# Performance work log

Hardware: AMD Instinct MI355X
Metric: run time of the kernel (lower is better)

Reference implementation:

```python
import jax, jax.numpy as jnp
import numpy as np

S = 4  # spixel_downsize


def _shift2d(x, oy, ox):
    # out[..., y, x] = x[..., y - oy, x - ox] if in-bounds else 0 (zero pad)
    pad = [(0, 0)] * (x.ndim - 2) + [(S, S), (S, S)]
    xp = jnp.pad(x, pad)
    h, w = x.shape[-2], x.shape[-1]
    return xp[..., S - oy:S - oy + h, S - ox:S - ox + w]


def _valid_mask(h, w, oy, ox):
    ys = jnp.arange(h)
    xs = jnp.arange(w)
    my = (ys - oy >= 0) & (ys - oy < h)
    mx = (xs - ox >= 0) & (xs - ox < w)
    return my[:, None] & mx[None, :]


def _conv3d(x, w, stride, pad):
    return jax.lax.conv_general_dilated(
        x, w, window_strides=stride, padding=[(p, p) for p in pad],
        dimension_numbers=('NCDHW', 'OIDHW', 'NCDHW'))


def _basic(x, w, stride, pad):
    # BasicConv: Conv3d(bias=False) + BN(identity at init) + ReLU
    return jax.nn.relu(_conv3d(x, w, stride, pad))


def setup_inputs() -> dict:
    key = jax.random.key(0)
    ks = jax.random.split(key, 8)
    cv = jax.random.normal(ks[0], (1, 8, 24, 128, 256), jnp.float32)
    sp = jax.random.uniform(ks[1], (1, 9, 128, 256), jnp.float32)
    xy = jax.random.normal(ks[2], (1, 2, 128, 256), jnp.float32)
    w_stem = jax.random.normal(ks[3], (16, 72, 1, 1, 1), jnp.float32) * 0.05
    w1a = jax.random.normal(ks[4], (32, 16, 3, 2, 2), jnp.float32) * 0.05
    w1b = jax.random.normal(ks[5], (32, 32, 3, 1, 1), jnp.float32) * 0.05
    w2a = jax.random.normal(ks[6], (64, 32, 3, 2, 2), jnp.float32) * 0.05
    w2b = jax.random.normal(ks[7], (64, 64, 3, 1, 1), jnp.float32) * 0.05
    return dict(cv=cv, sp=sp, xy=xy, w_stem=w_stem, w1a=w1a, w1b=w1b, w2a=w2a, w2b=w2b)


def reference(cv, sp, xy, w_stem, w1a, w1b, w2a, w2b):
    b, c, d, h, w = cv.shape
    feats, probs = [], []
    uv0 = jnp.zeros((b, 2, h, w), cv.dtype)
    # 9 shifted neighbors; neighbor k shifts by (S*((k//3)-1), S*((k%3)-1)).
    # All uv writes in the original target slot 0 and sequentially overwrite;
    for k in range(9):
        oy = S * ((k // 3) - 1)
        ox = S * ((k % 3) - 1)
        p = _shift2d(sp[:, k], oy, ox)                      # (b,h,w), zeros outside
        probs.append(p)
        feats.append(_shift2d(cv, oy, ox) * p[:, None, None])  # (b,c,d,h,w)
        u = _shift2d(xy, oy, ox) * p[:, None]               # (b,2,h,w)
        mask = _valid_mask(h, w, oy, ox)[None, None]
        uv0 = jnp.where(mask, u, uv0)
    # (b, c, 9, d, h, w) -> (b, 9c, d, h, w), matching torch reshape order
    feat = jnp.stack(feats, axis=2).reshape(b, c * 9, d, h, w)
    prob_sum = jnp.sum(jnp.stack(probs, axis=1), axis=1, keepdims=True)  # (b,1,h,w)
    tot = prob_sum.reshape(b, 1, h // S, S, w // S, S).mean((3, 5))      # avg_pool2d
    tot_up = jnp.repeat(jnp.repeat(tot, S, axis=2), S, axis=3)           # nearest upsample
    feat = feat / tot_up[:, :, None]                                     # (b,9c,d,h,w)
    feat = _basic(feat, w_stem, (1, 1, 1), (0, 0, 0))
    f1 = _basic(feat, w1a, (2, 2, 2), (1, 0, 0))
    f1 = _basic(f1, w1b, (1, 1, 1), (1, 0, 0))
    f2 = _basic(f1, w2a, (2, 2, 2), (1, 0, 0))
    f2 = _basic(f2, w2b, (1, 1, 1), (1, 0, 0))
    # uv.sum(2) == uv0 since only neighbor-slot 0 is written
    uv = uv0.reshape(b, 2, h // S, S, w // S, S).mean((3, 5)) / tot      # (b,2,h/S,w/S)
    return f1, f2, uv.reshape(b, 2, -1)
```

## Files before the change

### kernel.cpp

```cpp
#include <hip/hip_runtime.h>

#define HH 128
#define WW 256
#define HW (HH * WW)

#define OFF_TOT   0
#define OFF_WT    2048
#define WT_STEM   0
#define WT_1A     1152
#define WT_1B     7296
#define WT_2A     10368
#define WT_2B     34944
#define OFF_STEM  49280
#define OFF_F1A   12632192
#define OFF_F1N   15777920
#define OFF_F2A   49280

__global__ __launch_bounds__(256) void k_pre(
    const float* __restrict__ sp, const float* __restrict__ xy,
    const float* __restrict__ wstem, const float* __restrict__ w1a,
    const float* __restrict__ w1b, const float* __restrict__ w2a,
    const float* __restrict__ w2b,
    float* __restrict__ tot, float* __restrict__ uv_out, float* __restrict__ wt)
{
  int gid = blockIdx.x * 256 + threadIdx.x;
  if (gid < 1152) { int o = gid & 15, r = gid >> 4; int ci = r / 9, k = r - ci * 9;
    wt[WT_STEM + gid] = wstem[o * 72 + ci * 9 + k]; }
  if (gid < 6144) { int o = gid & 31, ci = (gid >> 5) & 15, tp = gid >> 9;
    wt[WT_1A + gid] = w1a[o * 192 + ci * 12 + tp]; }
  if (gid < 3072) { int o = gid & 31, ci = (gid >> 5) & 31, kd = gid >> 10;
    wt[WT_1B + gid] = w1b[(o * 32 + ci) * 3 + kd]; }
  if (gid < 24576) { int o = gid & 63, ci = (gid >> 6) & 31, tp = gid >> 11;
    wt[WT_2A + gid] = w2a[o * 384 + ci * 12 + tp]; }
  if (gid < 12288) { int o = gid & 63, ci = (gid >> 6) & 63, kd = gid >> 12;
    wt[WT_2B + gid] = w2b[(o * 64 + ci) * 3 + kd]; }
  if (gid < 8192) {
    int cell = gid >> 2, q = gid & 3;
    int Y = cell >> 6, X = cell & 63;
    float tsum = 0.f, u0 = 0.f, u1 = 0.f;
    int y = Y * 4 + q;
#pragma unroll
    for (int j = 0; j < 4; ++j) {
      int x = X * 4 + j;
      float psum = 0.f;
#pragma unroll
      for (int k = 0; k < 9; ++k) {
        int oy = 4 * ((k / 3) - 1), ox = 4 * ((k % 3) - 1);
        int sy = y - oy, sx = x - ox;
        if (sy >= 0 && sy < HH && sx >= 0 && sx < WW)
          psum += sp[k * HW + sy * WW + sx];
      }
      tsum += psum;
      int oy = (y >= 4) ? 4 : 0;
      int ox = (x >= 4) ? 4 : 0;
      int kk = (oy ? 2 : 1) * 3 + (ox ? 2 : 1);
      int sy = y - oy, sx = x - ox;
      float p = sp[kk * HW + sy * WW + sx];
      u0 += xy[sy * WW + sx] * p;
      u1 += xy[HW + sy * WW + sx] * p;
    }
    tsum += __shfl_xor(tsum, 1); tsum += __shfl_xor(tsum, 2);
    u0 += __shfl_xor(u0, 1); u0 += __shfl_xor(u0, 2);
    u1 += __shfl_xor(u1, 1); u1 += __shfl_xor(u1, 2);
    if (q == 0) {
      float t = tsum * (1.f / 16.f);
      tot[cell] = t;
      float inv = 1.f / t;
      uv_out[cell] = u0 * (1.f / 16.f) * inv;
      uv_out[2048 + cell] = u1 * (1.f / 16.f) * inv;
    }
  }
}

__global__ __launch_bounds__(256) void k_stem(
    const float* __restrict__ cv, const float* __restrict__ sp,
    const float* __restrict__ wt, const float* __restrict__ tot,
    float* __restrict__ out)
{
  __shared__ float wl[1152];
  for (int i = threadIdx.x; i < 1152; i += 256) wl[i] = wt[i];
  __syncthreads();
  int x0 = blockIdx.x * 128 + 2 * (threadIdx.x & 63);
  int y  = blockIdx.y * 4 + (threadIdx.x >> 6);
  int d  = blockIdx.z;
  float2 p2[9]; int off[9];
#pragma unroll
  for (int k = 0; k < 9; ++k) {
    int oy = 4 * ((k / 3) - 1), ox = 4 * ((k % 3) - 1);
    int sy = y - oy, sx = x0 - ox;
    bool v = (sy >= 0) && (sy < HH) && (sx >= 0) && (sx < WW - 1);
    int syc = v ? sy : 0, sxc = v ? sx : 0;
    off[k] = syc * WW + sxc;
    float2 t = *(const float2*)(sp + k * HW + off[k]);
    p2[k].x = v ? t.x : 0.f;
    p2[k].y = v ? t.y : 0.f;
  }
  float acc[16][2];
#pragma unroll
  for (int o = 0; o < 16; ++o) { acc[o][0] = 0.f; acc[o][1] = 0.f; }
  const float* cvd = cv + (size_t)d * HW;
  float2 cb[2][9];
#pragma unroll
  for (int k = 0; k < 9; ++k) cb[0][k] = *(const float2*)(cvd + off[k]);
#pragma unroll
  for (int ci = 0; ci < 8; ++ci) {
    if (ci < 7) {
#pragma unroll
      for (int k = 0; k < 9; ++k)
        cb[(ci + 1) & 1][k] = *(const float2*)(cvd + (size_t)(ci + 1) * 24 * HW + off[k]);
    }
#pragma unroll
    for (int k = 0; k < 9; ++k) {
      float t0 = cb[ci & 1][k].x * p2[k].x;
      float t1 = cb[ci & 1][k].y * p2[k].y;
      const float* wb = &wl[(ci * 9 + k) * 16];
      float wv[16];
#pragma unroll
      for (int q = 0; q < 4; ++q) *(float4*)&wv[q * 4] = *(const float4*)(wb + q * 4);
#pragma unroll
      for (int o = 0; o < 16; ++o) {
        acc[o][0] += wv[o] * t0;
        acc[o][1] += wv[o] * t1;
      }
    }
  }
  float inv = 1.f / tot[(y >> 2) * 64 + (x0 >> 2)];
  float* op = out + (((size_t)d * HH + y) * WW + x0) * 16;
#pragma unroll
  for (int p = 0; p < 2; ++p)
#pragma unroll
    for (int q = 0; q < 4; ++q) {
      float4 v;
      v.x = fmaxf(acc[q * 4 + 0][p] * inv, 0.f);
      v.y = fmaxf(acc[q * 4 + 1][p] * inv, 0.f);
      v.z = fmaxf(acc[q * 4 + 2][p] * inv, 0.f);
      v.w = fmaxf(acc[q * 4 + 3][p] * inv, 0.f);
      *(float4*)(op + p * 16 + q * 4) = v;
    }
}

__global__ __launch_bounds__(256, 1) void k_conv1a(
    const float* __restrict__ in, const float* __restrict__ wt,
    float* __restrict__ out)
{
  __shared__ float wl[3072];
  int og = blockIdx.z;
  for (int i = threadIdx.x; i < 3072; i += 256) {
    int o = i & 15, ci = (i >> 4) & 15, tap = i >> 8;
    wl[i] = wt[tap * 512 + ci * 32 + og * 16 + o];
  }
  __syncthreads();
  int tx = threadIdx.x & 31;
  int ty = threadIdx.x >> 5;
  int yo = blockIdx.x * 8 + ty;
  int dz = blockIdx.y;
  float acc[16][4];
#pragma unroll
  for (int o = 0; o < 16; ++o)
#pragma unroll
    for (int p = 0; p < 4; ++p) acc[o][p] = 0.f;
  for (int kd = 0; kd < 3; ++kd) {
    int d = 2 * dz - 1 + kd;
    if (d < 0 || d >= 24) continue;
#pragma unroll
    for (int ky = 0; ky < 2; ++ky) {
      int y = 2 * yo + ky;
      const float* base = in + (((size_t)d * 128 + y) * 256 + 8 * tx) * 16;
#pragma unroll
      for (int kx = 0; kx < 2; ++kx) {
        float ib[64];
#pragma unroll
        for (int p = 0; p < 4; ++p) {
          const float4* ip = (const float4*)(base + (2 * p + kx) * 16);
#pragma unroll
          for (int q = 0; q < 4; ++q) {
            float4 t = ip[q];
            ib[p * 16 + q * 4 + 0] = t.x; ib[p * 16 + q * 4 + 1] = t.y;
            ib[p * 16 + q * 4 + 2] = t.z; ib[p * 16 + q * 4 + 3] = t.w;
          }
        }
        const float* wtap = &wl[((kd * 2 + ky) * 2 + kx) * 256];
#pragma unroll
        for (int ci = 0; ci < 16; ++ci) {
          float wv[16];
#pragma unroll
          for (int q = 0; q < 4; ++q)
            *(float4*)&wv[q * 4] = *(const float4*)(wtap + ci * 16 + q * 4);
          float a0 = ib[0 * 16 + ci];
          float a1 = ib[1 * 16 + ci];
          float a2 = ib[2 * 16 + ci];
          float a3 = ib[3 * 16 + ci];
#pragma unroll
          for (int o = 0; o < 16; ++o) {
            acc[o][0] += wv[o] * a0;
            acc[o][1] += wv[o] * a1;
            acc[o][2] += wv[o] * a2;
            acc[o][3] += wv[o] * a3;
          }
        }
      }
    }
  }
  float* op = out + (((size_t)dz * 64 + yo) * 128 + 4 * tx) * 32 + og * 16;
#pragma unroll
  for (int p = 0; p < 4; ++p)
#pragma unroll
    for (int q = 0; q < 4; ++q) {
      float4 v;
      v.x = fmaxf(acc[q * 4 + 0][p], 0.f);
      v.y = fmaxf(acc[q * 4 + 1][p], 0.f);
      v.z = fmaxf(acc[q * 4 + 2][p], 0.f);
      v.w = fmaxf(acc[q * 4 + 3][p], 0.f);
      *(float4*)(op + p * 32 + q * 4) = v;
    }
}

__global__ __launch_bounds__(256) void k_conv1b(
    const float* __restrict__ in, const float* __restrict__ wt,
    float* __restrict__ outn, float* __restrict__ outc)
{
  __shared__ float wl[3072];
  for (int i = threadIdx.x; i < 3072; i += 256) wl[i] = wt[i];
  __syncthreads();
  int tid = threadIdx.x;
  int xo = (blockIdx.x & 1) * 64 + (tid & 63);
  int yo = (blockIdx.x >> 1) * 4 + (tid >> 6);
  int dz = blockIdx.y, og = blockIdx.z;
  float acc[16];
#pragma unroll
  for (int o = 0; o < 16; ++o) acc[o] = 0.f;
  for (int kd = 0; kd < 3; ++kd) {
    int d = dz - 1 + kd;
    if (d < 0 || d >= 12) continue;
    float iv[32];
    const float4* ip = (const float4*)(in + (((size_t)d * 64 + yo) * 128 + xo) * 32);
#pragma unroll
    for (int q = 0; q < 8; ++q) {
      float4 v = ip[q];
      iv[q * 4 + 0] = v.x; iv[q * 4 + 1] = v.y;
      iv[q * 4 + 2] = v.z; iv[q * 4 + 3] = v.w;
    }
    const float* wk = &wl[kd * 1024 + og * 16];
#pragma unroll
    for (int ci = 0; ci < 32; ++ci) {
      const float* wb = wk + ci * 32;
      float wv[16];
#pragma unroll
      for (int q = 0; q < 4; ++q) *(float4*)&wv[q * 4] = *(const float4*)(wb + q * 4);
#pragma unroll
      for (int o = 0; o < 16; ++o) acc[o] += wv[o] * iv[ci];
    }
  }
  float* onp = outn + (((size_t)dz * 64 + yo) * 128 + xo) * 32 + og * 16;
#pragma unroll
  for (int q = 0; q < 4; ++q) {
    float4 v;
    v.x = fmaxf(acc[q * 4 + 0], 0.f);
    v.y = fmaxf(acc[q * 4 + 1], 0.f);
    v.z = fmaxf(acc[q * 4 + 2], 0.f);
    v.w = fmaxf(acc[q * 4 + 3], 0.f);
    *(float4*)(onp + q * 4) = v;
  }
#pragma unroll
  for (int o = 0; o < 16; ++o)
    outc[((size_t)((og * 16 + o) * 12 + dz) * 64 + yo) * 128 + xo] = fmaxf(acc[o], 0.f);
}

__global__ __launch_bounds__(256) void k_conv2a(
    const float* __restrict__ in, const float* __restrict__ wt,
    float* __restrict__ out)
{
  __shared__ float wl[3072];
  int og = blockIdx.z;
  for (int i = threadIdx.x; i < 3072; i += 256) {
    int o = i & 7, ci = (i >> 3) & 31, tap = i >> 8;
    wl[i] = wt[tap * 2048 + ci * 64 + og * 8 + o];
  }
  __syncthreads();
  int xo = threadIdx.x & 63;
  int yo = blockIdx.x * 4 + (threadIdx.x >> 6);
  int dz = blockIdx.y;
  float acc[8];
#pragma unroll
  for (int o = 0; o < 8; ++o) acc[o] = 0.f;
  for (int kd = 0; kd < 3; ++kd) {
    int d = 2 * dz - 1 + kd;
    if (d < 0 || d >= 12) continue;
#pragma unroll
    for (int ky = 0; ky < 2; ++ky) {
      int y = 2 * yo + ky;
      float ib[64];
      const float4* ip = (const float4*)(in + (((size_t)d * 64 + y) * 128 + 2 * xo) * 32);
#pragma unroll
      for (int q = 0; q < 16; ++q) {
        float4 t = ip[q];
        ib[q * 4] = t.x; ib[q * 4 + 1] = t.y; ib[q * 4 + 2] = t.z; ib[q * 4 + 3] = t.w;
      }
#pragma unroll
      for (int kx = 0; kx < 2; ++kx) {
        const float* wtap = &wl[((kd * 2 + ky) * 2 + kx) * 256];
#pragma unroll
        for (int ci = 0; ci < 32; ++ci) {
          const float* wb = wtap + ci * 8;
          float wv[8];
          *(float4*)&wv[0] = *(const float4*)wb;
          *(float4*)&wv[4] = *(const float4*)(wb + 4);
          float a = ib[kx * 32 + ci];
#pragma unroll
          for (int o = 0; o < 8; ++o) acc[o] += wv[o] * a;
        }
      }
    }
  }
  float* op = out + (((size_t)dz * 32 + yo) * 64 + xo) * 64 + og * 8;
  float4 v0, v1;
  v0.x = fmaxf(acc[0], 0.f); v0.y = fmaxf(acc[1], 0.f);
  v0.z = fmaxf(acc[2], 0.f); v0.w = fmaxf(acc[3], 0.f);
  v1.x = fmaxf(acc[4], 0.f); v1.y = fmaxf(acc[5], 0.f);
  v1.z = fmaxf(acc[6], 0.f); v1.w = fmaxf(acc[7], 0.f);
  *(float4*)op = v0; *(float4*)(op + 4) = v1;
}

__global__ __launch_bounds__(256) void k_conv2b(
    const float* __restrict__ in, const float* __restrict__ wt,
    float* __restrict__ out)
{
  __shared__ float wl[1536];
  int og = blockIdx.z;
  for (int i = threadIdx.x; i < 1536; i += 256) {
    int o = i & 7, ci = (i >> 3) & 63, kd = i >> 9;
    wl[i] = wt[kd * 4096 + ci * 64 + og * 8 + o];
  }
  __syncthreads();
  int xo = threadIdx.x & 63;
  int yo = blockIdx.x * 4 + (threadIdx.x >> 6);
  int dz = blockIdx.y;
  float acc[8];
#pragma unroll
  for (int o = 0; o < 8; ++o) acc[o] = 0.f;
  for (int kd = 0; kd < 3; ++kd) {
    int d = dz - 1 + kd;
    if (d < 0 || d >= 6) continue;
    float ib[64];
    const float4* ip = (const float4*)(in + (((size_t)d * 32 + yo) * 64 + xo) * 64);
#pragma unroll
    for (int q = 0; q < 16; ++q) {
      float4 t = ip[q];
      ib[q * 4] = t.x; ib[q * 4 + 1] = t.y; ib[q * 4 + 2] = t.z; ib[q * 4 + 3] = t.w;
    }
    const float* wk = &wl[kd * 512];
#pragma unroll
    for (int ci = 0; ci < 64; ++ci) {
      const float* wb = wk + ci * 8;
      float wv[8];
      *(float4*)&wv[0] = *(const float4*)wb;
      *(float4*)&wv[4] = *(const float4*)(wb + 4);
      float a = ib[ci];
#pragma unroll
      for (int o = 0; o < 8; ++o) acc[o] += wv[o] * a;
    }
  }
#pragma unroll
  for (int o = 0; o < 8; ++o)
    out[((size_t)((og * 8 + o) * 6 + dz) * 32 + yo) * 64 + xo] = fmaxf(acc[o], 0.f);
}

extern "C" void kernel_launch(void* const* d_in, const int* in_sizes, int n_in,
                              void* d_out, int out_size, void* d_ws, size_t ws_size,
                              hipStream_t stream) {
  const float* cv    = (const float*)d_in[0];
  const float* sp    = (const float*)d_in[1];
  const float* xy    = (const float*)d_in[2];
  const float* wstem = (const float*)d_in[3];
  const float* w1a   = (const float*)d_in[4];
  const float* w1b   = (const float*)d_in[5];
  const float* w2a   = (const float*)d_in[6];
  const float* w2b   = (const float*)d_in[7];
  float* out = (float*)d_out;
  float* out_f1 = out;
  float* out_f2 = out + 3145728;
  float* out_uv = out + 3145728 + 786432;

  float* ws = (float*)d_ws;
  float* t_tot  = ws + OFF_TOT;
  float* wt     = ws + OFF_WT;
  float* t_stem = ws + OFF_STEM;
  float* t_f1a  = ws + OFF_F1A;
  float* t_f1n  = ws + OFF_F1N;
  float* t_f2a  = ws + OFF_F2A;

  k_pre<<<96, 256, 0, stream>>>(sp, xy, wstem, w1a, w1b, w2a, w2b,
                                t_tot, out_uv, wt);
  k_stem<<<dim3(2, 32, 24), 256, 0, stream>>>(cv, sp, wt + WT_STEM, t_tot, t_stem);
  k_conv1a<<<dim3(8, 12, 2), 256, 0, stream>>>(t_stem, wt + WT_1A, t_f1a);
  k_conv1b<<<dim3(32, 12, 2), 256, 0, stream>>>(t_f1a, wt + WT_1B, t_f1n, out_f1);
  k_conv2a<<<dim3(8, 6, 8), 256, 0, stream>>>(t_f1n, wt + WT_2A, t_f2a);
  k_conv2b<<<dim3(8, 6, 8), 256, 0, stream>>>(t_f2a, wt + WT_2B, out_f2);
}
```

Baseline: 172.7 us.

## Process two rows per thread in stem to share shifted cost-volume loads

Each stem thread now computes two output rows four apart, so the nine shifted neighbor reads of the cost volume overlap and only 12 distinct float2 loads per channel are needed instead of 18. Weight values loaded from shared memory are also reused across both rows. The grid is halved in y to match. This doubles accumulator registers (64 floats) and the prefetch buffers, which may lower occupancy.

```diff
diff --git a/kernel.cpp b/kernel.cpp
--- a/kernel.cpp
+++ b/kernel.cpp
@@ -80,63 +80,89 @@
   __shared__ float wl[1152];
   for (int i = threadIdx.x; i < 1152; i += 256) wl[i] = wt[i];
   __syncthreads();
-  int x0 = blockIdx.x * 128 + 2 * (threadIdx.x & 63);
-  int y  = blockIdx.y * 4 + (threadIdx.x >> 6);
+  int tx = threadIdx.x & 63;
+  int ty = threadIdx.x >> 6;
+  int x0 = blockIdx.x * 128 + 2 * tx;
+  int ya = blockIdx.y * 8 + ty;
   int d  = blockIdx.z;
-  float2 p2[9]; int off[9];
-#pragma unroll
-  for (int k = 0; k < 9; ++k) {
-    int oy = 4 * ((k / 3) - 1), ox = 4 * ((k % 3) - 1);
-    int sy = y - oy, sx = x0 - ox;
-    bool v = (sy >= 0) && (sy < HH) && (sx >= 0) && (sx < WW - 1);
-    int syc = v ? sy : 0, sxc = v ? sx : 0;
-    off[k] = syc * WW + sxc;
-    float2 t = *(const float2*)(sp + k * HW + off[k]);
-    p2[k].x = v ? t.x : 0.f;
-    p2[k].y = v ? t.y : 0.f;
-  }
-  float acc[16][2];
-#pragma unroll
-  for (int o = 0; o < 16; ++o) { acc[o][0] = 0.f; acc[o][1] = 0.f; }
+  float2 p2[2][9];
+#pragma unroll
+  for (int ry = 0; ry < 2; ++ry) {
+    int r = ya + 4 * ry;
+#pragma unroll
+    for (int k = 0; k < 9; ++k) {
+      int oy = 4 * ((k / 3) - 1), ox = 4 * ((k % 3) - 1);
+      int sy = r - oy, sx = x0 - ox;
+      bool v = (sy >= 0) && (sy < HH) && (sx >= 0) && (sx <= WW - 2);
+      int syc = v ? sy : 0, sxc = v ? sx : 0;
+      float2 t = *(const float2*)(sp + k * HW + syc * WW + sxc);
+      p2[ry][k].x = v ? t.x : 0.f;
+      p2[ry][k].y = v ? t.y : 0.f;
+    }
+  }
+  int coff[12];
+#pragma unroll
+  for (int m = 0; m < 4; ++m) {
+    int r = ya - 4 + 4 * m; r = r < 0 ? 0 : (r >= HH ? HH - 1 : r);
+#pragma unroll
+    for (int jx = 0; jx < 3; ++jx) {
+      int c = x0 - 4 + 4 * jx; c = c < 0 ? 0 : (c > WW - 2 ? WW - 2 : c);
+      coff[m * 3 + jx] = r * WW + c;
+    }
+  }
+  float acc[16][2][2];
+#pragma unroll
+  for (int o = 0; o < 16; ++o)
+#pragma unroll
+    for (int ry = 0; ry < 2; ++ry) { acc[o][ry][0] = 0.f; acc[o][ry][1] = 0.f; }
   const float* cvd = cv + (size_t)d * HW;
-  float2 cb[2][9];
-#pragma unroll
-  for (int k = 0; k < 9; ++k) cb[0][k] = *(const float2*)(cvd + off[k]);
+  float2 cb[2][12];
+#pragma unroll
+  for (int i = 0; i < 12; ++i) cb[0][i] = *(const float2*)(cvd + coff[i]);
 #pragma unroll
   for (int ci = 0; ci < 8; ++ci) {
     if (ci < 7) {
 #pragma unroll
-      for (int k = 0; k < 9; ++k)
-        cb[(ci + 1) & 1][k] = *(const float2*)(cvd + (size_t)(ci + 1) * 24 * HW + off[k]);
+      for (int i = 0; i < 12; ++i)
+        cb[(ci + 1) & 1][i] = *(const float2*)(cvd + (size_t)(ci + 1) * 24 * HW + coff[i]);
     }
 #pragma unroll
     for (int k = 0; k < 9; ++k) {
-      float t0 = cb[ci & 1][k].x * p2[k].x;
-      float t1 = cb[ci & 1][k].y * p2[k].y;
+      int kr = k / 3, kc = k - kr * 3;
       const float* wb = &wl[(ci * 9 + k) * 16];
       float wv[16];
 #pragma unroll
       for (int q = 0; q < 4; ++q) *(float4*)&wv[q * 4] = *(const float4*)(wb + q * 4);
 #pragma unroll
-      for (int o = 0; o < 16; ++o) {
-        acc[o][0] += wv[o] * t0;
-        acc[o][1] += wv[o] * t1;
-      }
-    }
-  }
-  float inv = 1.f / tot[(y >> 2) * 64 + (x0 >> 2)];
-  float* op = out + (((size_t)d * HH + y) * WW + x0) * 16;
-#pragma unroll
-  for (int p = 0; p < 2; ++p)
-#pragma unroll
-    for (int q = 0; q < 4; ++q) {
-      float4 v;
-      v.x = fmaxf(acc[q * 4 + 0][p] * inv, 0.f);
-      v.y = fmaxf(acc[q * 4 + 1][p] * inv, 0.f);
-      v.z = fmaxf(acc[q * 4 + 2][p] * inv, 0.f);
-      v.w = fmaxf(acc[q * 4 + 3][p] * inv, 0.f);
-      *(float4*)(op + p * 16 + q * 4) = v;
-    }
+      for (int ry = 0; ry < 2; ++ry) {
+        float2 c2 = cb[ci & 1][((2 - kr) + ry) * 3 + (2 - kc)];
+        float t0 = c2.x * p2[ry][k].x;
+        float t1 = c2.y * p2[ry][k].y;
+#pragma unroll
+        for (int o = 0; o < 16; ++o) {
+          acc[o][ry][0] += wv[o] * t0;
+          acc[o][ry][1] += wv[o] * t1;
+        }
+      }
+    }
+  }
+#pragma unroll
+  for (int ry = 0; ry < 2; ++ry) {
+    int r = ya + 4 * ry;
+    float inv = 1.f / tot[(r >> 2) * 64 + (x0 >> 2)];
+    float* op = out + (((size_t)d * HH + r) * WW + x0) * 16;
+#pragma unroll
+    for (int p = 0; p < 2; ++p)
+#pragma unroll
+      for (int q = 0; q < 4; ++q) {
+        float4 v;
+        v.x = fmaxf(acc[q * 4 + 0][ry][p] * inv, 0.f);
+        v.y = fmaxf(acc[q * 4 + 1][ry][p] * inv, 0.f);
+        v.z = fmaxf(acc[q * 4 + 2][ry][p] * inv, 0.f);
+        v.w = fmaxf(acc[q * 4 + 3][ry][p] * inv, 0.f);
+        *(float4*)(op + p * 16 + q * 4) = v;
+      }
+  }
 }
 
 __global__ __launch_bounds__(256, 1) void k_conv1a(
@@ -391,7 +417,7 @@
 
   k_pre<<<96, 256, 0, stream>>>(sp, xy, wstem, w1a, w1b, w2a, w2b,
                                 t_tot, out_uv, wt);
-  k_stem<<<dim3(2, 32, 24), 256, 0, stream>>>(cv, sp, wt + WT_STEM, t_tot, t_stem);
+  k_stem<<<dim3(2, 16, 24), 256, 0, stream>>>(cv, sp, wt + WT_STEM, t_tot, t_stem);
   k_conv1a<<<dim3(8, 12, 2), 256, 0, stream>>>(t_stem, wt + WT_1A, t_f1a);
   k_conv1b<<<dim3(32, 12, 2), 256, 0, stream>>>(t_f1a, wt + WT_1B, t_f1n, out_f1);
   k_conv2a<<<dim3(8, 6, 8), 256, 0, stream>>>(t_f1n, wt + WT_2A, t_f2a);
```

New measurement: 181.5 us. +5.1%, slower.
